# Kernel tuning notes

Measured on AMD Instinct MI355X. Metric: run time of the kernel, lower is better.

Reference implementation:

```python
import jax, jax.numpy as jnp
import numpy as np

B, T = 8192, 26
V, E, H, L = 23, 100, 128, 64  # vocab, emb dim, GRU hidden, latent; LSTM hidden = E


def setup_inputs() -> dict:
    key = jax.random.key(0)
    ks = jax.random.split(key, 16)
    rn = lambda k, shape, scale=0.1: (jax.random.normal(k, shape, jnp.float32) * scale)
    emb = rn(ks[0], (V, E)).at[0].set(0.0)  # padding_idx=0 row zeroed
    return {
        "z": jax.random.normal(ks[1], (B, L), jnp.float32),
        "x_in": jax.random.randint(ks[2], (B, T), 0, V),
        "emb": emb,
        "fc_z_w": rn(ks[3], (H, L)), "fc_z_b": rn(ks[4], (H,)),
        "gru_wih": rn(ks[5], (3 * H, E)), "gru_whh": rn(ks[6], (3 * H, H)),
        "gru_bih": rn(ks[7], (3 * H,)), "gru_bhh": rn(ks[8], (3 * H,)),
        "lstm_wih": rn(ks[9], (4 * E, H)), "lstm_whh": rn(ks[10], (4 * E, E)),
        "lstm_bih": rn(ks[11], (4 * E,)), "lstm_bhh": rn(ks[12], (4 * E,)),
        "out_w": rn(ks[13], (V, E)), "out_b": rn(ks[14], (V,)),
    }


def _gru(e, h0, Wih, Whh, bih, bhh):
    # e: (B,T,E); precompute input projections for all steps, scan over T.
    xg = jnp.einsum('bti,gi->btg', e, Wih) + bih  # (B,T,3H)

    def step(h, x):
        hg = h @ Whh.T + bhh
        xr, xz, xn = jnp.split(x, 3, axis=-1)
        hr, hz, hn = jnp.split(hg, 3, axis=-1)
        r = jax.nn.sigmoid(xr + hr)
        zg = jax.nn.sigmoid(xz + hz)
        n = jnp.tanh(xn + r * hn)
        h_new = (1.0 - zg) * n + zg * h
        return h_new, h_new

    _, ys = jax.lax.scan(step, h0, jnp.swapaxes(xg, 0, 1))  # (T,B,H)
    return jnp.swapaxes(ys, 0, 1)


def _lstm(x, h0, c0, Wih, Whh, bih, bhh):
    xg = jnp.einsum('bti,gi->btg', x, Wih) + bih  # (B,T,4E)

    def step(hc, xt):
        h, c = hc
        g = xt + h @ Whh.T + bhh
        i, f, gg, o = jnp.split(g, 4, axis=-1)
        c_new = jax.nn.sigmoid(f) * c + jax.nn.sigmoid(i) * jnp.tanh(gg)
        h_new = jax.nn.sigmoid(o) * jnp.tanh(c_new)
        return (h_new, c_new), h_new

    _, ys = jax.lax.scan(step, (h0, c0), jnp.swapaxes(xg, 0, 1))
    return jnp.swapaxes(ys, 0, 1)


def reference(z, x_in, emb, fc_z_w, fc_z_b, gru_wih, gru_whh, gru_bih, gru_bhh,
              lstm_wih, lstm_whh, lstm_bih, lstm_bhh, out_w, out_b):
    h0 = jnp.tanh(z @ fc_z_w.T + fc_z_b)            # (B,H)
    e = emb[x_in]                                    # (B,T,E)
    y = _gru(e, h0, gru_wih, gru_whh, gru_bih, gru_bhh)           # (B,T,H)
    zeros = jnp.zeros((z.shape[0], E), dtype=z.dtype)
    y = _lstm(y, zeros, zeros, lstm_wih, lstm_whh, lstm_bih, lstm_bhh)  # (B,T,E)
    logits = jnp.einsum('bte,ve->btv', y, out_w) + out_b          # (B,T,V)
    return logits
```

## Files before the change

kernel.cpp:

```cpp
#include <hip/hip_runtime.h>
#include <stdint.h>
#include <stddef.h>

#define BB 8192
#define TT 26
#define VV 23
#define EE 100
#define HH 128
#define LL 64

typedef __attribute__((ext_vector_type(8))) short bf16x8;
typedef __attribute__((ext_vector_type(4))) float f32x4;

#define MFMA(a, b, c) __builtin_amdgcn_mfma_f32_16x16x32_bf16((a), (b), (c), 0, 0, 0)

#define OFF_GRUW   0ull
#define OFF_TBL    98304ull
#define OFF_LSTMW  122880ull
#define OFF_OUTW   352256ull
#define OFF_FCZW   360448ull
#define OFF_LBIAS  376832ull
#define OFF_Y      379904ull

__device__ __forceinline__ void force_frag(bf16x8& v) { asm volatile("" : "+v"(v)); }

__device__ __forceinline__ unsigned short f2bf(float f) {
  union { float f; unsigned u; } v; v.f = f;
  unsigned u = v.u;
  return (unsigned short)((u + 0x7FFFu + ((u >> 16) & 1u)) >> 16);
}
__device__ __forceinline__ unsigned short f2bf_fast(float f) {
  union { float f; unsigned u; } v; v.f = f;
  return (unsigned short)((v.u + 0x8000u) >> 16);
}
#define LOG2E 1.4426950408889634f
__device__ __forceinline__ float sigm(float x) {
  return __builtin_amdgcn_rcpf(1.0f + __builtin_amdgcn_exp2f(-x * LOG2E));
}
__device__ __forceinline__ float tanh_(float x) {
  return __builtin_fmaf(-2.0f,
      __builtin_amdgcn_rcpf(1.0f + __builtin_amdgcn_exp2f(x * (2.0f * LOG2E))), 1.0f);
}

__global__ __launch_bounds__(256) void prep_kernel(
    const float* __restrict__ emb, const float* __restrict__ fc_z_w,
    const float* __restrict__ gru_wih, const float* __restrict__ gru_whh,
    const float* __restrict__ gru_bih,
    const float* __restrict__ lstm_wih, const float* __restrict__ lstm_whh,
    const float* __restrict__ lstm_bih, const float* __restrict__ lstm_bhh,
    const float* __restrict__ out_w,
    char* __restrict__ ws)
{
  int e = blockIdx.x * 256 + threadIdx.x;

  if (e < 49152) {
    int j = e & 7, lane = (e >> 3) & 63, kc = (e >> 9) & 3, ct = e >> 11;
    int n = ct * 16 + (lane & 15);
    int k = kc * 32 + ((lane >> 4) & 3) * 8 + j;
    *(unsigned short*)(ws + OFF_GRUW + (size_t)e * 2) = f2bf(gru_whh[n * HH + k]);
    return;
  }
  e -= 49152;
  if (e < 12288) {
    int j = e & 7, lane = (e >> 3) & 63, ct = e >> 9;
    int n = ct * 16 + (lane & 15);
    int k = ((lane >> 4) & 3) * 8 + j;
    float v = 0.0f;
    if (k < VV) {
      float s0 = 0.f, s1 = 0.f, s2 = 0.f, s3 = 0.f;
      const float* ep = emb + k * EE;
      const float* wp = gru_wih + n * EE;
#pragma unroll 5
      for (int m = 0; m < EE; m += 4) {
        s0 += ep[m] * wp[m];     s1 += ep[m + 1] * wp[m + 1];
        s2 += ep[m + 2] * wp[m + 2]; s3 += ep[m + 3] * wp[m + 3];
      }
      v = gru_bih[n] + ((s0 + s1) + (s2 + s3));
    }
    *(unsigned short*)(ws + OFF_TBL + (size_t)e * 2) = f2bf(v);
    return;
  }
  e -= 12288;
  if (e < 114688) {
    int j = e & 7, lane = (e >> 3) & 63, kc = (e >> 9) & 7, ct = e >> 12;
    int row = ct * 16 + (lane & 15);
    int g = row / 112, c = row % 112;
    int q = (lane >> 4) & 3;
    float v = 0.0f;
    if (c < EE) {
      if (kc < 4) {
        int k = kc * 32 + q * 8 + j;
        v = lstm_wih[(g * EE + c) * HH + k];
      } else {
        int k = (kc - 4) * 32 + q * 8 + j;
        if (k < EE) v = lstm_whh[(g * EE + c) * EE + k];
      }
    }
    *(unsigned short*)(ws + OFF_LSTMW + (size_t)e * 2) = f2bf(v);
    return;
  }
  e -= 114688;
  if (e < 4096) {
    int j = e & 7, lane = (e >> 3) & 63, kc = (e >> 9) & 3, ct = e >> 11;
    int n = ct * 16 + (lane & 15);
    int k = kc * 32 + ((lane >> 4) & 3) * 8 + j;
    float v = (n < VV && k < EE) ? out_w[n * EE + k] : 0.0f;
    *(unsigned short*)(ws + OFF_OUTW + (size_t)e * 2) = f2bf(v);
    return;
  }
  e -= 4096;
  if (e < 8192) {
    int j = e & 7, lane = (e >> 3) & 63, kc = (e >> 9) & 1, ct = e >> 10;
    int n = ct * 16 + (lane & 15);
    int k = kc * 32 + ((lane >> 4) & 3) * 8 + j;
    *(unsigned short*)(ws + OFF_FCZW + (size_t)e * 2) = f2bf(fc_z_w[n * LL + k]);
    return;
  }
  e -= 8192;
  if (e < 448) {
    int g = e / 112, c = e % 112;
    float v = (c < EE) ? (lstm_bih[g * EE + c] + lstm_bhh[g * EE + c]) : 0.0f;
    *(float*)(ws + OFF_LBIAS + (size_t)e * 4) = v;
  }
}

__global__ __launch_bounds__(512, 2) void gru_kernel(
    const float* __restrict__ z, const int* __restrict__ x_in,
    const float* __restrict__ fc_z_b, const float* __restrict__ gru_bhh,
    const unsigned short* __restrict__ gruw, const unsigned short* __restrict__ tbl,
    const unsigned short* __restrict__ fczw, unsigned short* __restrict__ yout)
{
  __shared__ unsigned short hfrag[2][2][2048];
  __shared__ unsigned char idx_lds[TT * 32];
  const int tid  = threadIdx.x;
  const int wv   = tid >> 6;
  const int lane = tid & 63;
  const int l15  = lane & 15;
  const int q    = (lane >> 4) & 3;
  const int blk  = blockIdx.x;

  for (int i = tid; i < TT * 32; i += 512) {
    int t = i >> 5, r = i & 31;
    idx_lds[i] = (unsigned char)x_in[(blk * 32 + r) * TT + t];
  }

  bf16x8 gw[3][4], tw[3];
#pragma unroll
  for (int g = 0; g < 3; g++) {
    int ct = g * 8 + wv;
#pragma unroll
    for (int kc = 0; kc < 4; kc++) {
      gw[g][kc] = *(const bf16x8*)(gruw + (size_t)(ct * 4 + kc) * 512 + lane * 8);
      force_frag(gw[g][kc]);
    }
    tw[g] = *(const bf16x8*)(tbl + (size_t)ct * 512 + lane * 8);
    force_frag(tw[g]);
  }
  const int col = wv * 16 + l15;
  const float b_r = gru_bhh[0 * HH + col];
  const float b_z = gru_bhh[1 * HH + col];
  const float b_n = gru_bhh[2 * HH + col];
  const int wbase = (col >> 5) * 512 + ((col >> 3) & 3) * 128 + (col & 7);

  float h[2][4];
  {
    bf16x8 fw0 = *(const bf16x8*)(fczw + (size_t)(wv * 2 + 0) * 512 + lane * 8);
    bf16x8 fw1 = *(const bf16x8*)(fczw + (size_t)(wv * 2 + 1) * 512 + lane * 8);
    float fzb = fc_z_b[col];
#pragma unroll
    for (int s = 0; s < 2; s++) {
      const float* zp = z + (size_t)(blk * 32 + s * 16 + l15) * LL + q * 8;
      f32x4 z0 = *(const f32x4*)(zp);
      f32x4 z1 = *(const f32x4*)(zp + 4);
      f32x4 z2 = *(const f32x4*)(zp + 32);
      f32x4 z3 = *(const f32x4*)(zp + 36);
      bf16x8 za0, za1;
#pragma unroll
      for (int j = 0; j < 4; j++) {
        za0[j]     = (short)f2bf(z0[j]);
        za0[4 + j] = (short)f2bf(z1[j]);
        za1[j]     = (short)f2bf(z2[j]);
        za1[4 + j] = (short)f2bf(z3[j]);
      }
      f32x4 acc = {fzb, fzb, fzb, fzb};
      acc = MFMA(za0, fw0, acc);
      acc = MFMA(za1, fw1, acc);
#pragma unroll
      for (int i = 0; i < 4; i++) {
        h[s][i] = tanh_(acc[i]);
        hfrag[0][s][wbase + (q * 4 + i) * 8] = f2bf_fast(h[s][i]);
      }
    }
  }
  __syncthreads();

  const int xs = wv >> 2, xk = wv & 3;
  int cur = 0;
  for (int t = 0; t < TT; t++) {
    if (t > 0) {
      bf16x8 yv = *(const bf16x8*)&hfrag[cur][xs][xk * 512 + lane * 8];
      *(bf16x8*)(yout + ((size_t)((blk * 2 + xs) * TT + (t - 1)) * 4 + xk) * 512 + lane * 8) = yv;
    }
    int nb = cur ^ 1;
#pragma unroll
    for (int s = 0; s < 2; s++) {
      int iv = idx_lds[t * 32 + s * 16 + l15];
      bf16x8 oh;
#pragma unroll
      for (int j = 0; j < 8; j++)
        oh[j] = (short)((iv == q * 8 + j) ? 0x3F80 : 0);

      f32x4 ar  = {b_r, b_r, b_r, b_r};
      f32x4 az  = {b_z, b_z, b_z, b_z};
      f32x4 ahn = {b_n, b_n, b_n, b_n};
      f32x4 axn = {0.0f, 0.0f, 0.0f, 0.0f};
      ar  = MFMA(oh, tw[0], ar);
      az  = MFMA(oh, tw[1], az);
      axn = MFMA(oh, tw[2], axn);

      bf16x8 a[4];
#pragma unroll
      for (int kc = 0; kc < 4; kc++)
        a[kc] = *(const bf16x8*)&hfrag[cur][s][kc * 512 + lane * 8];
#pragma unroll
      for (int kc = 0; kc < 4; kc++) {
        ar  = MFMA(a[kc], gw[0][kc], ar);
        az  = MFMA(a[kc], gw[1][kc], az);
        ahn = MFMA(a[kc], gw[2][kc], ahn);
      }
#pragma unroll
      for (int i = 0; i < 4; i++) {
        float r  = sigm(ar[i]);
        float zg = sigm(az[i]);
        float n  = tanh_(__builtin_fmaf(r, ahn[i], axn[i]));
        h[s][i] = __builtin_fmaf(zg, h[s][i] - n, n);
        hfrag[nb][s][wbase + (q * 4 + i) * 8] = f2bf_fast(h[s][i]);
      }
    }
    __syncthreads();
    cur = nb;
  }
  {
    bf16x8 yv = *(const bf16x8*)&hfrag[cur][xs][xk * 512 + lane * 8];
    *(bf16x8*)(yout + ((size_t)((blk * 2 + xs) * TT + (TT - 1)) * 4 + xk) * 512 + lane * 8) = yv;
  }
}

__global__ __launch_bounds__(512, 2) void lstm_kernel(
    const unsigned short* __restrict__ lstmw, const float* __restrict__ lbias,
    const unsigned short* __restrict__ ybuf,
    const float* __restrict__ out_b, const unsigned short* __restrict__ outw,
    float* __restrict__ out)
{
  __shared__ unsigned short hbuf[2][2][2048];
  const int tid  = threadIdx.x;
  const int wv   = tid >> 6;
  const int lane = tid & 63;
  const int l15  = lane & 15;
  const int q    = (lane >> 4) & 3;
  const int blk  = blockIdx.x;

  for (int i = tid; i < 2 * 2 * 2048; i += 512)
    ((unsigned short*)hbuf)[i] = 0;

  if (wv < 7) {
    bf16x8 lw[4][8];
#pragma unroll
    for (int g = 0; g < 4; g++)
#pragma unroll
      for (int kc = 0; kc < 8; kc++) {
        lw[g][kc] = *(const bf16x8*)(lstmw + (size_t)((g * 7 + wv) * 8 + kc) * 512 + lane * 8);
        force_frag(lw[g][kc]);
      }
    const int col = wv * 16 + l15;
    float b[4];
#pragma unroll
    for (int g = 0; g < 4; g++) b[g] = lbias[g * 112 + col];
    const int wbase = (col >> 5) * 512 + ((col >> 3) & 3) * 128 + (col & 7);
    float c[2][4] = {{0, 0, 0, 0}, {0, 0, 0, 0}};
    __syncthreads();

    for (int p = 0; p <= TT; p++) {
      if (p < TT) {
        bf16x8 ya[2][4];
#pragma unroll
        for (int s = 0; s < 2; s++)
#pragma unroll
          for (int kc = 0; kc < 4; kc++)
            ya[s][kc] = *(const bf16x8*)(ybuf + ((size_t)((blk * 2 + s) * TT + p) * 4 + kc) * 512 + lane * 8);

#pragma unroll
        for (int s = 0; s < 2; s++) {
          bf16x8 ha[4];
#pragma unroll
          for (int kc = 0; kc < 4; kc++)
            ha[kc] = *(const bf16x8*)&hbuf[p & 1][s][kc * 512 + lane * 8];
          f32x4 ai = {b[0], b[0], b[0], b[0]};
          f32x4 af = {b[1], b[1], b[1], b[1]};
          f32x4 ag = {b[2], b[2], b[2], b[2]};
          f32x4 ao = {b[3], b[3], b[3], b[3]};
#pragma unroll
          for (int kc = 0; kc < 4; kc++) {
            ai = MFMA(ha[kc], lw[0][kc + 4], ai);
            af = MFMA(ha[kc], lw[1][kc + 4], af);
            ag = MFMA(ha[kc], lw[2][kc + 4], ag);
            ao = MFMA(ha[kc], lw[3][kc + 4], ao);
          }
#pragma unroll
          for (int kc = 0; kc < 4; kc++) {
            ai = MFMA(ya[s][kc], lw[0][kc], ai);
            af = MFMA(ya[s][kc], lw[1][kc], af);
            ag = MFMA(ya[s][kc], lw[2][kc], ag);
            ao = MFMA(ya[s][kc], lw[3][kc], ao);
          }
#pragma unroll
          for (int i = 0; i < 4; i++) {
            float ii = sigm(ai[i]), ff = sigm(af[i]);
            float gg = tanh_(ag[i]), oo = sigm(ao[i]);
            float cn = __builtin_fmaf(ff, c[s][i], ii * gg);
            c[s][i] = cn;
            hbuf[(p + 1) & 1][s][wbase + (q * 4 + i) * 8] = f2bf_fast(oo * tanh_(cn));
          }
        }
      }
      __syncthreads();
    }
  } else {
    bf16x8 ow[2][4];
#pragma unroll
    for (int ct = 0; ct < 2; ct++)
#pragma unroll
      for (int kc = 0; kc < 4; kc++) {
        ow[ct][kc] = *(const bf16x8*)(outw + (size_t)(ct * 4 + kc) * 512 + lane * 8);
        force_frag(ow[ct][kc]);
      }
    float ob[2];
#pragma unroll
    for (int ct = 0; ct < 2; ct++) {
      int cv = ct * 16 + l15;
      ob[ct] = (cv < VV) ? out_b[cv] : 0.0f;
    }
    __syncthreads();

    for (int p = 0; p <= TT; p++) {
      if (p >= 1) {
        const int t = p - 1;
#pragma unroll
        for (int s = 0; s < 2; s++) {
          bf16x8 ha[4];
#pragma unroll
          for (int kc = 0; kc < 4; kc++)
            ha[kc] = *(const bf16x8*)&hbuf[p & 1][s][kc * 512 + lane * 8];
#pragma unroll
          for (int ct = 0; ct < 2; ct++) {
            f32x4 acc = {ob[ct], ob[ct], ob[ct], ob[ct]};
#pragma unroll
            for (int kc = 0; kc < 4; kc++)
              acc = MFMA(ha[kc], ow[ct][kc], acc);
            int cv = ct * 16 + l15;
            if (cv < VV) {
#pragma unroll
              for (int i = 0; i < 4; i++) {
                int rowg = blk * 32 + s * 16 + q * 4 + i;
                out[((size_t)rowg * TT + t) * VV + cv] = acc[i];
              }
            }
          }
        }
      }
      __syncthreads();
    }
  }
}

extern "C" void kernel_launch(void* const* d_in, const int* in_sizes, int n_in,
                              void* d_out, int out_size, void* d_ws, size_t ws_size,
                              hipStream_t stream) {
  (void)in_sizes; (void)n_in; (void)out_size; (void)ws_size;
  const float* z        = (const float*)d_in[0];
  const int*   x_in     = (const int*)  d_in[1];
  const float* emb      = (const float*)d_in[2];
  const float* fc_z_w   = (const float*)d_in[3];
  const float* fc_z_b   = (const float*)d_in[4];
  const float* gru_wih  = (const float*)d_in[5];
  const float* gru_whh  = (const float*)d_in[6];
  const float* gru_bih  = (const float*)d_in[7];
  const float* gru_bhh  = (const float*)d_in[8];
  const float* lstm_wih = (const float*)d_in[9];
  const float* lstm_whh = (const float*)d_in[10];
  const float* lstm_bih = (const float*)d_in[11];
  const float* lstm_bhh = (const float*)d_in[12];
  const float* out_w    = (const float*)d_in[13];
  const float* out_b    = (const float*)d_in[14];
  char*  ws  = (char*)d_ws;
  float* out = (float*)d_out;

  const unsigned short* gruw  = (const unsigned short*)(ws + OFF_GRUW);
  const unsigned short* tblp  = (const unsigned short*)(ws + OFF_TBL);
  const unsigned short* lstmw = (const unsigned short*)(ws + OFF_LSTMW);
  const unsigned short* outw  = (const unsigned short*)(ws + OFF_OUTW);
  const unsigned short* fczw  = (const unsigned short*)(ws + OFF_FCZW);
  const float*          lbias = (const float*)(ws + OFF_LBIAS);
  unsigned short*       ybuf  = (unsigned short*)(ws + OFF_Y);

  prep_kernel<<<738, 256, 0, stream>>>(emb, fc_z_w, gru_wih, gru_whh, gru_bih,
                                       lstm_wih, lstm_whh, lstm_bih, lstm_bhh,
                                       out_w, ws);
  gru_kernel<<<256, 512, 0, stream>>>(z, x_in, fc_z_b, gru_bhh,
                                      gruw, tblp, fczw, ybuf);
  lstm_kernel<<<256, 512, 0, stream>>>(lstmw, lbias, ybuf, out_b, outw, out);
}
```

Baseline: 207.9 us.

## Split table prep, halve GRU batch per block, prefetch LSTM input projection

The embedding-projection table is moved into its own kernel, which stages emb and the gru_wih rows in shared memory so they are not re-read from global memory per element. The GRU kernel now handles 16 sequences per block with 512 blocks and launch bounds raised to 4 blocks per CU, trading work per block for more parallelism across CUs. The LSTM loop issues the next step's y loads and input-projection MFMAs after the current gate math, so only the recurrent MFMAs sit on the serial path. The tradeoffs are an extra kernel launch, more register pressure in the GRU kernel, and a different y layout that the LSTM kernel must read correctly.

```diff
diff --git a/kernel.cpp b/kernel.cpp
--- a/kernel.cpp
+++ b/kernel.cpp
@@ -42,14 +42,46 @@
       __builtin_amdgcn_rcpf(1.0f + __builtin_amdgcn_exp2f(x * (2.0f * LOG2E))), 1.0f);
 }
 
-__global__ __launch_bounds__(256) void prep_kernel(
-    const float* __restrict__ emb, const float* __restrict__ fc_z_w,
-    const float* __restrict__ gru_wih, const float* __restrict__ gru_whh,
-    const float* __restrict__ gru_bih,
+__global__ __launch_bounds__(512) void prep_table_kernel(
+    const float* __restrict__ emb, const float* __restrict__ gru_wih,
+    const float* __restrict__ gru_bih, char* __restrict__ ws)
+{
+  __shared__ float emb_s[VV * EE];
+  __shared__ float wih_s[16 * EE];
+  __shared__ float bih_s[16];
+  const int tid = threadIdx.x;
+  const int ct  = blockIdx.x;
+  const int n0  = ct * 16;
+
+  for (int i = tid; i < VV * EE; i += 512) emb_s[i] = emb[i];
+  for (int i = tid; i < 16 * EE; i += 512) wih_s[i] = gru_wih[n0 * EE + i];
+  if (tid < 16) bih_s[tid] = gru_bih[n0 + tid];
+  __syncthreads();
+
+  const int j    = tid & 7;
+  const int lane = (tid >> 3) & 63;
+  const int n16  = lane & 15;
+  const int k    = ((lane >> 4) & 3) * 8 + j;
+  float v = 0.0f;
+  if (k < VV) {
+    const float* ep = emb_s + k * EE;
+    const float* wp = wih_s + n16 * EE;
+    float s0 = 0.f, s1 = 0.f, s2 = 0.f, s3 = 0.f;
+#pragma unroll 5
+    for (int m = 0; m < EE; m += 4) {
+      s0 += ep[m] * wp[m];         s1 += ep[m + 1] * wp[m + 1];
+      s2 += ep[m + 2] * wp[m + 2]; s3 += ep[m + 3] * wp[m + 3];
+    }
+    v = bih_s[n16] + ((s0 + s1) + (s2 + s3));
+  }
+  *(unsigned short*)(ws + OFF_TBL + (size_t)(ct * 512 + tid) * 2) = f2bf(v);
+}
+
+__global__ __launch_bounds__(256) void prep_main_kernel(
+    const float* __restrict__ fc_z_w, const float* __restrict__ gru_whh,
     const float* __restrict__ lstm_wih, const float* __restrict__ lstm_whh,
     const float* __restrict__ lstm_bih, const float* __restrict__ lstm_bhh,
-    const float* __restrict__ out_w,
-    char* __restrict__ ws)
+    const float* __restrict__ out_w, char* __restrict__ ws)
 {
   int e = blockIdx.x * 256 + threadIdx.x;
 
@@ -61,26 +93,6 @@
     return;
   }
   e -= 49152;
-  if (e < 12288) {
-    int j = e & 7, lane = (e >> 3) & 63, ct = e >> 9;
-    int n = ct * 16 + (lane & 15);
-    int k = ((lane >> 4) & 3) * 8 + j;
-    float v = 0.0f;
-    if (k < VV) {
-      float s0 = 0.f, s1 = 0.f, s2 = 0.f, s3 = 0.f;
-      const float* ep = emb + k * EE;
-      const float* wp = gru_wih + n * EE;
-#pragma unroll 5
-      for (int m = 0; m < EE; m += 4) {
-        s0 += ep[m] * wp[m];     s1 += ep[m + 1] * wp[m + 1];
-        s2 += ep[m + 2] * wp[m + 2]; s3 += ep[m + 3] * wp[m + 3];
-      }
-      v = gru_bih[n] + ((s0 + s1) + (s2 + s3));
-    }
-    *(unsigned short*)(ws + OFF_TBL + (size_t)e * 2) = f2bf(v);
-    return;
-  }
-  e -= 12288;
   if (e < 114688) {
     int j = e & 7, lane = (e >> 3) & 63, kc = (e >> 9) & 7, ct = e >> 12;
     int row = ct * 16 + (lane & 15);
@@ -124,14 +136,14 @@
   }
 }
 
-__global__ __launch_bounds__(512, 2) void gru_kernel(
+__global__ __launch_bounds__(512, 4) void gru_kernel(
     const float* __restrict__ z, const int* __restrict__ x_in,
     const float* __restrict__ fc_z_b, const float* __restrict__ gru_bhh,
     const unsigned short* __restrict__ gruw, const unsigned short* __restrict__ tbl,
     const unsigned short* __restrict__ fczw, unsigned short* __restrict__ yout)
 {
-  __shared__ unsigned short hfrag[2][2][2048];
-  __shared__ unsigned char idx_lds[TT * 32];
+  __shared__ unsigned short hfrag[2][2048];
+  __shared__ unsigned char idx_lds[TT * 16];
   const int tid  = threadIdx.x;
   const int wv   = tid >> 6;
   const int lane = tid & 63;
@@ -139,9 +151,9 @@
   const int q    = (lane >> 4) & 3;
   const int blk  = blockIdx.x;
 
-  for (int i = tid; i < TT * 32; i += 512) {
-    int t = i >> 5, r = i & 31;
-    idx_lds[i] = (unsigned char)x_in[(blk * 32 + r) * TT + t];
+  for (int i = tid; i < TT * 16; i += 512) {
+    int t = i >> 4, r = i & 15;
+    idx_lds[i] = (unsigned char)x_in[(blk * 16 + r) * TT + t];
   }
 
   bf16x8 gw[3][4], tw[3];
@@ -162,87 +174,81 @@
   const float b_n = gru_bhh[2 * HH + col];
   const int wbase = (col >> 5) * 512 + ((col >> 3) & 3) * 128 + (col & 7);
 
-  float h[2][4];
+  float h[4];
   {
     bf16x8 fw0 = *(const bf16x8*)(fczw + (size_t)(wv * 2 + 0) * 512 + lane * 8);
     bf16x8 fw1 = *(const bf16x8*)(fczw + (size_t)(wv * 2 + 1) * 512 + lane * 8);
+    const float* zp = z + (size_t)(blk * 16 + l15) * LL + q * 8;
+    f32x4 z0 = *(const f32x4*)(zp);
+    f32x4 z1 = *(const f32x4*)(zp + 4);
+    f32x4 z2 = *(const f32x4*)(zp + 32);
+    f32x4 z3 = *(const f32x4*)(zp + 36);
+    bf16x8 za0, za1;
+#pragma unroll
+    for (int j = 0; j < 4; j++) {
+      za0[j]     = (short)f2bf(z0[j]);
+      za0[4 + j] = (short)f2bf(z1[j]);
+      za1[j]     = (short)f2bf(z2[j]);
+      za1[4 + j] = (short)f2bf(z3[j]);
+    }
     float fzb = fc_z_b[col];
-#pragma unroll
-    for (int s = 0; s < 2; s++) {
-      const float* zp = z + (size_t)(blk * 32 + s * 16 + l15) * LL + q * 8;
-      f32x4 z0 = *(const f32x4*)(zp);
-      f32x4 z1 = *(const f32x4*)(zp + 4);
-      f32x4 z2 = *(const f32x4*)(zp + 32);
-      f32x4 z3 = *(const f32x4*)(zp + 36);
-      bf16x8 za0, za1;
-#pragma unroll
-      for (int j = 0; j < 4; j++) {
-        za0[j]     = (short)f2bf(z0[j]);
-        za0[4 + j] = (short)f2bf(z1[j]);
-        za1[j]     = (short)f2bf(z2[j]);
-        za1[4 + j] = (short)f2bf(z3[j]);
-      }
-      f32x4 acc = {fzb, fzb, fzb, fzb};
-      acc = MFMA(za0, fw0, acc);
-      acc = MFMA(za1, fw1, acc);
-#pragma unroll
-      for (int i = 0; i < 4; i++) {
-        h[s][i] = tanh_(acc[i]);
-        hfrag[0][s][wbase + (q * 4 + i) * 8] = f2bf_fast(h[s][i]);
-      }
+    f32x4 acc = {fzb, fzb, fzb, fzb};
+    acc = MFMA(za0, fw0, acc);
+    acc = MFMA(za1, fw1, acc);
+#pragma unroll
+    for (int i = 0; i < 4; i++) {
+      h[i] = tanh_(acc[i]);
+      hfrag[0][wbase + (q * 4 + i) * 8] = f2bf_fast(h[i]);
     }
   }
   __syncthreads();
 
-  const int xs = wv >> 2, xk = wv & 3;
   int cur = 0;
   for (int t = 0; t < TT; t++) {
-    if (t > 0) {
-      bf16x8 yv = *(const bf16x8*)&hfrag[cur][xs][xk * 512 + lane * 8];
-      *(bf16x8*)(yout + ((size_t)((blk * 2 + xs) * TT + (t - 1)) * 4 + xk) * 512 + lane * 8) = yv;
-    }
+    if (t > 0 && wv < 4) {
+      bf16x8 yv = *(const bf16x8*)((const char*)hfrag[cur] + wv * 1024 + lane * 16);
+      *(bf16x8*)(yout + ((size_t)(blk * TT + (t - 1)) * 4 + wv) * 512 + lane * 8) = yv;
+    }
+    int iv = idx_lds[t * 16 + l15];
+    bf16x8 oh;
+#pragma unroll
+    for (int j = 0; j < 8; j++)
+      oh[j] = (short)((iv == q * 8 + j) ? 0x3F80 : 0);
+
+    f32x4 ar  = {b_r, b_r, b_r, b_r};
+    f32x4 az  = {b_z, b_z, b_z, b_z};
+    f32x4 ahn = {b_n, b_n, b_n, b_n};
+    f32x4 axn = {0.0f, 0.0f, 0.0f, 0.0f};
+    ar  = MFMA(oh, tw[0], ar);
+    az  = MFMA(oh, tw[1], az);
+    axn = MFMA(oh, tw[2], axn);
+
+    bf16x8 a[4];
+#pragma unroll
+    for (int kc = 0; kc < 4; kc++)
+      a[kc] = *(const bf16x8*)((const char*)hfrag[cur] + kc * 1024 + lane * 16);
+#pragma unroll
+    for (int kc = 0; kc < 4; kc++) {
+      ar  = MFMA(a[kc], gw[0][kc], ar);
+      az  = MFMA(a[kc], gw[1][kc], az);
+      ahn = MFMA(a[kc], gw[2][kc], ahn);
+    }
+
     int nb = cur ^ 1;
 #pragma unroll
-    for (int s = 0; s < 2; s++) {
-      int iv = idx_lds[t * 32 + s * 16 + l15];
-      bf16x8 oh;
-#pragma unroll
-      for (int j = 0; j < 8; j++)
-        oh[j] = (short)((iv == q * 8 + j) ? 0x3F80 : 0);
-
-      f32x4 ar  = {b_r, b_r, b_r, b_r};
-      f32x4 az  = {b_z, b_z, b_z, b_z};
-      f32x4 ahn = {b_n, b_n, b_n, b_n};
-      f32x4 axn = {0.0f, 0.0f, 0.0f, 0.0f};
-      ar  = MFMA(oh, tw[0], ar);
-      az  = MFMA(oh, tw[1], az);
-      axn = MFMA(oh, tw[2], axn);
-
-      bf16x8 a[4];
-#pragma unroll
-      for (int kc = 0; kc < 4; kc++)
-        a[kc] = *(const bf16x8*)&hfrag[cur][s][kc * 512 + lane * 8];
-#pragma unroll
-      for (int kc = 0; kc < 4; kc++) {
-        ar  = MFMA(a[kc], gw[0][kc], ar);
-        az  = MFMA(a[kc], gw[1][kc], az);
-        ahn = MFMA(a[kc], gw[2][kc], ahn);
-      }
-#pragma unroll
-      for (int i = 0; i < 4; i++) {
-        float r  = sigm(ar[i]);
-        float zg = sigm(az[i]);
-        float n  = tanh_(__builtin_fmaf(r, ahn[i], axn[i]));
-        h[s][i] = __builtin_fmaf(zg, h[s][i] - n, n);
-        hfrag[nb][s][wbase + (q * 4 + i) * 8] = f2bf_fast(h[s][i]);
-      }
+    for (int i = 0; i < 4; i++) {
+      float r  = sigm(ar[i]);
+      float zg = sigm(az[i]);
+      float n  = tanh_(__builtin_fmaf(r, ahn[i], axn[i]));
+      h[i] = __builtin_fmaf(zg, h[i] - n, n);
+      hfrag[nb][wbase + (q * 4 + i) * 8] = f2bf_fast(h[i]);
     }
     __syncthreads();
     cur = nb;
   }
-  {
-    bf16x8 yv = *(const bf16x8*)&hfrag[cur][xs][xk * 512 + lane * 8];
-    *(bf16x8*)(yout + ((size_t)((blk * 2 + xs) * TT + (TT - 1)) * 4 + xk) * 512 + lane * 8) = yv;
+  if (wv < 4) {
+    bf16x8 yv = *(const bf16x8*)((const char*)hfrag[cur] + wv * 1024 + lane * 16);
+    *(bf16x8*)(yout + ((size_t)(blk * TT + (TT - 1)) * 4 + wv) * 512 + lane * 8) = yv;
   }
 }
 
@@ -280,51 +286,72 @@
     float c[2][4] = {{0, 0, 0, 0}, {0, 0, 0, 0}};
     __syncthreads();
 
-    for (int p = 0; p <= TT; p++) {
-      if (p < TT) {
-        bf16x8 ya[2][4];
-#pragma unroll
-        for (int s = 0; s < 2; s++)
-#pragma unroll
-          for (int kc = 0; kc < 4; kc++)
-            ya[s][kc] = *(const bf16x8*)(ybuf + ((size_t)((blk * 2 + s) * TT + p) * 4 + kc) * 512 + lane * 8);
-
-#pragma unroll
-        for (int s = 0; s < 2; s++) {
-          bf16x8 ha[4];
-#pragma unroll
-          for (int kc = 0; kc < 4; kc++)
-            ha[kc] = *(const bf16x8*)&hbuf[p & 1][s][kc * 512 + lane * 8];
-          f32x4 ai = {b[0], b[0], b[0], b[0]};
-          f32x4 af = {b[1], b[1], b[1], b[1]};
-          f32x4 ag = {b[2], b[2], b[2], b[2]};
-          f32x4 ao = {b[3], b[3], b[3], b[3]};
-#pragma unroll
-          for (int kc = 0; kc < 4; kc++) {
-            ai = MFMA(ha[kc], lw[0][kc + 4], ai);
-            af = MFMA(ha[kc], lw[1][kc + 4], af);
-            ag = MFMA(ha[kc], lw[2][kc + 4], ag);
-            ao = MFMA(ha[kc], lw[3][kc + 4], ao);
-          }
-#pragma unroll
-          for (int kc = 0; kc < 4; kc++) {
-            ai = MFMA(ya[s][kc], lw[0][kc], ai);
-            af = MFMA(ya[s][kc], lw[1][kc], af);
-            ag = MFMA(ya[s][kc], lw[2][kc], ag);
-            ao = MFMA(ya[s][kc], lw[3][kc], ao);
-          }
-#pragma unroll
-          for (int i = 0; i < 4; i++) {
-            float ii = sigm(ai[i]), ff = sigm(af[i]);
-            float gg = tanh_(ag[i]), oo = sigm(ao[i]);
-            float cn = __builtin_fmaf(ff, c[s][i], ii * gg);
-            c[s][i] = cn;
-            hbuf[(p + 1) & 1][s][wbase + (q * 4 + i) * 8] = f2bf_fast(oo * tanh_(cn));
-          }
+    f32x4 yacc[2][4];
+#pragma unroll
+    for (int s = 0; s < 2; s++) {
+      bf16x8 ya[4];
+#pragma unroll
+      for (int kc = 0; kc < 4; kc++)
+        ya[kc] = *(const bf16x8*)(ybuf + ((size_t)((blk * 2 + s) * TT + 0) * 4 + kc) * 512 + lane * 8);
+#pragma unroll
+      for (int g = 0; g < 4; g++) yacc[s][g] = (f32x4){b[g], b[g], b[g], b[g]};
+#pragma unroll
+      for (int kc = 0; kc < 4; kc++) {
+        yacc[s][0] = MFMA(ya[kc], lw[0][kc], yacc[s][0]);
+        yacc[s][1] = MFMA(ya[kc], lw[1][kc], yacc[s][1]);
+        yacc[s][2] = MFMA(ya[kc], lw[2][kc], yacc[s][2]);
+        yacc[s][3] = MFMA(ya[kc], lw[3][kc], yacc[s][3]);
+      }
+    }
+
+    for (int p = 0; p < TT; p++) {
+      const int pn = (p + 1 < TT) ? (p + 1) : (TT - 1);
+#pragma unroll
+      for (int s = 0; s < 2; s++) {
+        bf16x8 ha[4];
+#pragma unroll
+        for (int kc = 0; kc < 4; kc++)
+          ha[kc] = *(const bf16x8*)&hbuf[p & 1][s][kc * 512 + lane * 8];
+#pragma unroll
+        for (int kc = 0; kc < 4; kc++) {
+          yacc[s][0] = MFMA(ha[kc], lw[0][kc + 4], yacc[s][0]);
+          yacc[s][1] = MFMA(ha[kc], lw[1][kc + 4], yacc[s][1]);
+          yacc[s][2] = MFMA(ha[kc], lw[2][kc + 4], yacc[s][2]);
+          yacc[s][3] = MFMA(ha[kc], lw[3][kc + 4], yacc[s][3]);
         }
       }
+      bf16x8 yan[2][4];
+#pragma unroll
+      for (int s = 0; s < 2; s++)
+#pragma unroll
+        for (int kc = 0; kc < 4; kc++)
+          yan[s][kc] = *(const bf16x8*)(ybuf + ((size_t)((blk * 2 + s) * TT + pn) * 4 + kc) * 512 + lane * 8);
+#pragma unroll
+      for (int s = 0; s < 2; s++) {
+#pragma unroll
+        for (int i = 0; i < 4; i++) {
+          float ii = sigm(yacc[s][0][i]), ff = sigm(yacc[s][1][i]);
+          float gg = tanh_(yacc[s][2][i]), oo = sigm(yacc[s][3][i]);
+          float cn = __builtin_fmaf(ff, c[s][i], ii * gg);
+          c[s][i] = cn;
+          hbuf[(p + 1) & 1][s][wbase + (q * 4 + i) * 8] = f2bf_fast(oo * tanh_(cn));
+        }
+      }
+#pragma unroll
+      for (int s = 0; s < 2; s++) {
+#pragma unroll
+        for (int g = 0; g < 4; g++) yacc[s][g] = (f32x4){b[g], b[g], b[g], b[g]};
+#pragma unroll
+        for (int kc = 0; kc < 4; kc++) {
+          yacc[s][0] = MFMA(yan[s][kc], lw[0][kc], yacc[s][0]);
+          yacc[s][1] = MFMA(yan[s][kc], lw[1][kc], yacc[s][1]);
+          yacc[s][2] = MFMA(yan[s][kc], lw[2][kc], yacc[s][2]);
+          yacc[s][3] = MFMA(yan[s][kc], lw[3][kc], yacc[s][3]);
+        }
+      }
       __syncthreads();
     }
+    __syncthreads();
   } else {
     bf16x8 ow[2][4];
 #pragma unroll
@@ -403,10 +430,10 @@
   const float*          lbias = (const float*)(ws + OFF_LBIAS);
   unsigned short*       ybuf  = (unsigned short*)(ws + OFF_Y);
 
-  prep_kernel<<<738, 256, 0, stream>>>(emb, fc_z_w, gru_wih, gru_whh, gru_bih,
-                                       lstm_wih, lstm_whh, lstm_bih, lstm_bhh,
-                                       out_w, ws);
-  gru_kernel<<<256, 512, 0, stream>>>(z, x_in, fc_z_b, gru_bhh,
+  prep_main_kernel<<<690, 256, 0, stream>>>(fc_z_w, gru_whh, lstm_wih, lstm_whh,
+                                            lstm_bih, lstm_bhh, out_w, ws);
+  prep_table_kernel<<<24, 512, 0, stream>>>(emb, gru_wih, gru_bih, ws);
+  gru_kernel<<<512, 512, 0, stream>>>(z, x_in, fc_z_b, gru_bhh,
                                       gruw, tblp, fczw, ybuf);
   lstm_kernel<<<256, 512, 0, stream>>>(lstmw, lbias, ybuf, out_b, outw, out);
 }
```

Result: faster. 190.1 us (-8.6%).
